# Performance work log

Hardware: AMD Instinct MI355X
Metric: run time of the kernel (lower is better)

The kernel has to match this reference:

```python
import jax, jax.numpy as jnp
import numpy as np

B, L, C = 4, 4096, 2048
NH, K = 32, 16
F = C // NH  # head_dim = 64
LR = 1.0     # config.inner_net_lr
EPS = 1e-6


def setup_inputs() -> dict:
    key = jax.random.key(0)
    ks = jax.random.split(key, 8)
    s = 0.02
    return {
        "hidden_states": jax.random.normal(ks[0], (B, L, C), jnp.float32),
        "q_w": jax.random.normal(ks[1], (C, C), jnp.float32) * s,
        "k_w": jax.random.normal(ks[2], (C, C), jnp.float32) * s,
        "v_w": jax.random.normal(ks[3], (C, C), jnp.float32) * s,
        "o_w": jax.random.normal(ks[4], (C, C), jnp.float32) * s,
        "lin_w": jax.random.normal(ks[5], (NH, 1, C), jnp.float32) * s,
        "lin_b": jnp.zeros((NH, 1), jnp.float32),
        "ln_w": jnp.ones((NH, F), jnp.float32),
        "ln_b": jnp.zeros((NH, F), jnp.float32),
        "W1": jax.random.normal(ks[6], (NH, F, F), jnp.float32) * s,
        "b1": jnp.zeros((NH, 1, F), jnp.float32),
    }


def _ln(z, g, b):
    # LayerNormFunction.forward over last dim (head_dim)
    mu = z.mean(-1, keepdims=True)
    var = jnp.mean((z - mu) ** 2, axis=-1, keepdims=True)
    x_hat = (z - mu) * jax.lax.rsqrt(var + EPS)
    return g * x_hat + b


def _ln_l2_bwd(z, target, g, b):
    # decoder_ln_bwd: grad of 0.5*||LN(z) - target||^2 w.r.t. z, fused LN fwd+bwd
    mu = z.mean(-1, keepdims=True)
    var = jnp.mean((z - mu) ** 2, axis=-1, keepdims=True)
    std = jnp.sqrt(var + EPS)
    x_hat = (z - mu) / std
    gy = (g * x_hat + b - target) * g  # grad_x_hat
    return (F * gy - gy.sum(-1, keepdims=True)
            - x_hat * (gy * x_hat).sum(-1, keepdims=True)) / (F * std)


def reference(hidden_states, q_w, k_w, v_w, o_w, lin_w, lin_b, ln_w, ln_b, W1, b1):
    nc = L // K  # number of inner chunks

    def proj(w):
        x = hidden_states @ w.T                      # [B,L,C]
        x = x.reshape(B, nc, K, NH, F)
        return jnp.moveaxis(x, 3, 1)                 # [B,NH,nc,K,F]

    XC, XB, XA = proj(q_w), proj(k_w), proj(v_w)

    # per-head ilr gate: vmap(F.linear) over heads, softplus activation
    Xr = hidden_states.reshape(B, nc, K, C)
    ilr = jax.nn.softplus(jnp.einsum('bnkc,hoc->bhnko', Xr, lin_w)
                          + lin_b[None, :, None, None, :])   # [B,NH,nc,K,1]
    token_idx = 1.0 / jnp.arange(1, K + 1, dtype=jnp.float32)
    coeff = (LR * token_idx)[None, None, None, :, None] * ilr / F  # [B,NH,nc,K,1]

    gamma = ln_w[None, :, None, :]  # [1,NH,1,F]
    beta = ln_b[None, :, None, :]
    mask = jnp.tril(jnp.ones((K, K), jnp.float32))

    W1_0 = jnp.broadcast_to(W1[None], (B, NH, F, F))
    b1_0 = jnp.broadcast_to(b1[None], (B, NH, 1, F))

    def step(carry, xs):
        W1s, b1s = carry
        xa, xb, xc, co = xs                 # [B,NH,K,F], co: [B,NH,K,1]
        Z1 = xb @ W1s + b1s                 # inner-net forward
        gZ = _ln_l2_bwd(Z1, xa - xb, gamma, beta)  # grad_l_wrt_Z1
        Attn1 = (xc @ jnp.swapaxes(xb, -1, -2)) * mask      # tril(XC XB^T) [B,NH,K,K]
        b1_bar = b1s - (co * mask) @ gZ                      # [B,NH,K,F]
        Z1_bar = xc @ W1s - (co * Attn1) @ gZ + b1_bar       # dual-form output
        co_last = co[:, :, -1:, :]                           # [B,NH,1,1]
        W1_new = W1s - jnp.swapaxes(co_last * xb, -1, -2) @ gZ
        b1_new = b1_bar[:, :, -1:, :]
        xcw = xc + _ln(Z1_bar, gamma, beta)
        return (W1_new, b1_new), xcw

    xs = tuple(jnp.moveaxis(t, 2, 0) for t in (XA, XB, XC, coeff))
    _, out = jax.lax.scan(step, (W1_0, b1_0), xs)   # out: [nc,B,NH,K,F]
    out = jnp.moveaxis(out, 0, 1)                    # [B,nc,NH,K,F]
    out = jnp.swapaxes(out, 2, 3).reshape(B, L, C)   # [B,L,C]
    return out @ o_w.T
```

## Files before the change

kernel.cpp:

```cpp
#include <hip/hip_runtime.h>
#include <hip/hip_bf16.h>

#define B_ 4
#define L_ 4096
#define C_ 2048
#define NH_ 32
#define K_ 16
#define F_ 64
#define NC_ 256
#define EPS_ 1e-6f

typedef _Float16 half8 __attribute__((ext_vector_type(8)));
typedef _Float16 half4 __attribute__((ext_vector_type(4)));
typedef float f32x4 __attribute__((ext_vector_type(4)));

__device__ __forceinline__ float red16(float v) {
  int x;
  x = __builtin_amdgcn_update_dpp(0, __builtin_bit_cast(int, v), 0xB1, 0xF, 0xF, true);
  v += __builtin_bit_cast(float, x);
  x = __builtin_amdgcn_update_dpp(0, __builtin_bit_cast(int, v), 0x4E, 0xF, 0xF, true);
  v += __builtin_bit_cast(float, x);
  x = __builtin_amdgcn_update_dpp(0, __builtin_bit_cast(int, v), 0x124, 0xF, 0xF, true);
  v += __builtin_bit_cast(float, x);
  x = __builtin_amdgcn_update_dpp(0, __builtin_bit_cast(int, v), 0x128, 0xF, 0xF, true);
  v += __builtin_bit_cast(float, x);
  return v;
}

__device__ __forceinline__ void gl_lds16(const _Float16* g, _Float16* l) {
  __builtin_amdgcn_global_load_lds(
      (const __attribute__((address_space(1))) void*)g,
      (__attribute__((address_space(3))) void*)l, 16, 0, 0);
}

__global__ __launch_bounds__(256) void cast_f16(const float* __restrict__ in,
                                                _Float16* __restrict__ out, int n8) {
  int i = blockIdx.x * 256 + threadIdx.x;
  if (i >= n8) return;
  const float4* ip = (const float4*)in;
  float4 a = ip[2*i], b = ip[2*i+1];
  half8 o;
  o[0]=(_Float16)a.x; o[1]=(_Float16)a.y; o[2]=(_Float16)a.z; o[3]=(_Float16)a.w;
  o[4]=(_Float16)b.x; o[5]=(_Float16)b.y; o[6]=(_Float16)b.z; o[7]=(_Float16)b.w;
  ((half8*)out)[i] = o;
}

#define TM 128
#define TN 128
#define TK 32

template<typename OT>
__global__ __launch_bounds__(256) void gemm_f16(
    const _Float16* __restrict__ A, const _Float16* __restrict__ Bm,
    OT* __restrict__ C, int M, int N, int Kd)
{
  __shared__ __align__(16) _Float16 As[TM*TK];
  __shared__ __align__(16) _Float16 Bs[TN*TK];
  const int t = threadIdx.x;
  const int lane = t & 63;
  const int bn = blockIdx.x, bm = blockIdx.y;
  const int w = t >> 6;
  const int wm = (w >> 1) * 64, wn = (w & 1) * 64;

  const _Float16* ga1 = A  + ((long)(bm*TM +      (t>>2)))*Kd + (t&3)*8;
  const _Float16* ga2 = A  + ((long)(bm*TM + 64 + (t>>2)))*Kd + (t&3)*8;
  const _Float16* gb1 = Bm + ((long)(bn*TN +      (t>>2)))*Kd + (t&3)*8;
  const _Float16* gb2 = Bm + ((long)(bn*TN + 64 + (t>>2)))*Kd + (t&3)*8;
  _Float16* la1 = As + (size_t)t*8;
  _Float16* la2 = As + (size_t)(t+256)*8;
  _Float16* lb1 = Bs + (size_t)t*8;
  _Float16* lb2 = Bs + (size_t)(t+256)*8;

  f32x4 acc[4][4];
#pragma unroll
  for (int i = 0; i < 4; ++i)
#pragma unroll
    for (int j = 0; j < 4; ++j) acc[i][j] = (f32x4){0.f,0.f,0.f,0.f};

  for (int k0 = 0; k0 < Kd; k0 += TK) {
    __syncthreads();
    gl_lds16(ga1 + k0, la1);
    gl_lds16(ga2 + k0, la2);
    gl_lds16(gb1 + k0, lb1);
    gl_lds16(gb2 + k0, lb2);
    __syncthreads();
    half8 af[4], bf[4];
#pragma unroll
    for (int i = 0; i < 4; ++i)
      af[i] = *(const half8*)(As + (size_t)(wm + i*16 + (lane&15))*TK + (lane>>4)*8);
#pragma unroll
    for (int j = 0; j < 4; ++j)
      bf[j] = *(const half8*)(Bs + (size_t)(wn + j*16 + (lane&15))*TK + (lane>>4)*8);
#pragma unroll
    for (int i = 0; i < 4; ++i)
#pragma unroll
      for (int j = 0; j < 4; ++j)
        acc[i][j] = __builtin_amdgcn_mfma_f32_16x16x32_f16(af[i], bf[j], acc[i][j], 0, 0, 0);
  }

  const int cr = (lane >> 4) * 4, cc = lane & 15;
#pragma unroll
  for (int i = 0; i < 4; ++i)
#pragma unroll
    for (int j = 0; j < 4; ++j)
#pragma unroll
      for (int r = 0; r < 4; ++r) {
        long row = (long)bm*TM + wm + i*16 + cr + r;
        long col = (long)bn*TN + wn + j*16 + cc;
        C[row*(long)N + col] = (OT)acc[i][j][r];
      }
}

__global__ __launch_bounds__(256) void ilr_kernel(
    const float* __restrict__ hid, const float* __restrict__ lin_w,
    const float* __restrict__ lin_b, float* __restrict__ coeff)
{
  const int t = threadIdx.x;
  const int lane = t & 63;
  const int w = t >> 6;
  const int row0 = blockIdx.x * 16 + w * 4;

  float4 hv[4][8];
#pragma unroll
  for (int r = 0; r < 4; ++r) {
    const float* hp = hid + (size_t)(row0 + r) * C_;
#pragma unroll
    for (int i = 0; i < 8; ++i) hv[r][i] = *(const float4*)(hp + i*256 + lane*4);
  }
  float res[4] = {0.f,0.f,0.f,0.f};
  for (int h = 0; h < NH_; ++h) {
    const float* wp = lin_w + (size_t)h * C_;
    float s[4] = {0.f,0.f,0.f,0.f};
#pragma unroll
    for (int i = 0; i < 8; ++i) {
      float4 wv = *(const float4*)(wp + i*256 + lane*4);
#pragma unroll
      for (int r = 0; r < 4; ++r)
        s[r] += hv[r][i].x*wv.x + hv[r][i].y*wv.y + hv[r][i].z*wv.z + hv[r][i].w*wv.w;
    }
#pragma unroll
    for (int o = 32; o > 0; o >>= 1)
#pragma unroll
      for (int r = 0; r < 4; ++r) s[r] += __shfl_xor(s[r], o, 64);
    if (lane == h) { res[0]=s[0]; res[1]=s[1]; res[2]=s[2]; res[3]=s[3]; }
  }
  if (lane < NH_) {
    float lb = lin_b[lane];
#pragma unroll
    for (int r = 0; r < 4; ++r) {
      int row = row0 + r;
      int b = row >> 12;
      int li = row & (L_ - 1);
      int k = li & (K_ - 1);
      float x = res[r] + lb;
      float sp = (x > 20.f) ? x : log1pf(expf(x));
      float v = (1.0f / (float)(k + 1)) * sp * (1.0f / (float)F_);
      coeff[((size_t)(b * NH_ + lane)) * L_ + li] = v;
    }
  }
}


struct Ck {
  half4 xbA[4], xcA[4], xaA[4];
  float co4[4], co15;
};

__device__ __forceinline__ void load_ck(
    Ck& c, const _Float16* Q, const _Float16* Kp, const _Float16* V,
    const float* co, size_t rowbase, int hoff, size_t cobase, int n, int q, int ln)
{
#pragma unroll
  for (int kt = 0; kt < 4; ++kt) {
    size_t idx = (rowbase + ln) * C_ + hoff + 16*kt + 4*q;
    c.xbA[kt] = *(const half4*)(Kp + idx);
    c.xcA[kt] = *(const half4*)(Q  + idx);
    c.xaA[kt] = *(const half4*)(V  + idx);
  }
#pragma unroll
  for (int r = 0; r < 4; ++r) c.co4[r] = co[cobase + (size_t)n*K_ + 4*q + r];
  c.co15 = co[cobase + (size_t)n*K_ + 15];
}

__global__ __launch_bounds__(64, 1) void scan_kernel(
    const _Float16* __restrict__ Q, const _Float16* __restrict__ Kp,
    const _Float16* __restrict__ V,
    const float* __restrict__ coeff, const float* __restrict__ W1g, const float* __restrict__ b1g,
    const float* __restrict__ ln_w, const float* __restrict__ ln_b,
    _Float16* __restrict__ OF)
{
  const int bh = blockIdx.x;
  const int b = bh >> 5, h = bh & 31;
  const int lane = threadIdx.x;
  const int q = lane >> 4, ln = lane & 15;
  const int hoff = h * F_;
  const size_t cobase = (size_t)bh * L_;
  const size_t brow = (size_t)b * L_;

  half4 Whi[4][4];
  f32x4 Wlo[4][4];
#pragma unroll
  for (int kt = 0; kt < 4; ++kt)
#pragma unroll
    for (int t = 0; t < 4; ++t) {
      half4 hv; f32x4 lv;
#pragma unroll
      for (int j = 0; j < 4; ++j) {
        float wv = W1g[(size_t)h*F_*F_ + (size_t)(16*kt + 4*q + j)*F_ + 16*t + ln];
        _Float16 hi = (_Float16)wv;
        hv[j] = hi; lv[j] = wv - (float)hi;
      }
      Whi[kt][t] = hv; Wlo[kt][t] = lv;
    }
  float b1r[4], gamt[4], bett[4];
#pragma unroll
  for (int t = 0; t < 4; ++t) {
    b1r[t]  = b1g[hoff + 16*t + ln];
    gamt[t] = ln_w[hoff + 16*t + ln];
    bett[t] = ln_b[hoff + 16*t + ln];
  }
  half4 maskA, maskI;
#pragma unroll
  for (int j = 0; j < 4; ++j) {
    maskA[j] = (_Float16)((4*q + j <= ln) ? 1.f : 0.f);
    maskI[j] = (_Float16)((4*q + j == ln) ? 1.f : 0.f);
  }
  const f32x4 zf4 = (f32x4){0.f, 0.f, 0.f, 0.f};

  auto body = [&](const Ck& ck, int n) {
    const size_t rowbase = brow + (size_t)n * K_;

    half4 Wlo16[4][4];
#pragma unroll
    for (int kt = 0; kt < 4; ++kt)
#pragma unroll
      for (int t = 0; t < 4; ++t) {
        half4 lv;
#pragma unroll
        for (int j = 0; j < 4; ++j) lv[j] = (_Float16)Wlo[kt][t][j];
        Wlo16[kt][t] = lv;
      }

    f32x4 tgD[4], xcsD[4];
    half4 xbT[4];
#pragma unroll
    for (int t = 0; t < 4; ++t) {
      half4 dd = ck.xaA[t] - ck.xbA[t];
      tgD[t]  = __builtin_amdgcn_mfma_f32_16x16x16f16(dd, maskI, zf4, 0, 0, 0);
      xcsD[t] = __builtin_amdgcn_mfma_f32_16x16x16f16(ck.xcA[t], maskI, zf4, 0, 0, 0);
      f32x4 x = __builtin_amdgcn_mfma_f32_16x16x16f16(ck.xbA[t], maskI, zf4, 0, 0, 0);
      half4 v;
#pragma unroll
      for (int r = 0; r < 4; ++r) v[r] = (_Float16)x[r];
      xbT[t] = v;
    }

    f32x4 za[4];
#pragma unroll
    for (int t = 0; t < 4; ++t) {
      f32x4 zh = (f32x4){b1r[t], b1r[t], b1r[t], b1r[t]};
      f32x4 zl = zf4;
#pragma unroll
      for (int kt = 0; kt < 4; ++kt) {
        zh = __builtin_amdgcn_mfma_f32_16x16x16f16(ck.xbA[kt], Whi[kt][t],   zh, 0, 0, 0);
        zl = __builtin_amdgcn_mfma_f32_16x16x16f16(ck.xbA[kt], Wlo16[kt][t], zl, 0, 0, 0);
      }
      za[t] = zh + zl;
    }

    f32x4 at0 = zf4, at1 = zf4;
    at0 = __builtin_amdgcn_mfma_f32_16x16x16f16(ck.xbA[0], ck.xcA[0], at0, 0, 0, 0);
    at0 = __builtin_amdgcn_mfma_f32_16x16x16f16(ck.xbA[1], ck.xcA[1], at0, 0, 0, 0);
    at1 = __builtin_amdgcn_mfma_f32_16x16x16f16(ck.xbA[2], ck.xcA[2], at1, 0, 0, 0);
    at1 = __builtin_amdgcn_mfma_f32_16x16x16f16(ck.xbA[3], ck.xcA[3], at1, 0, 0, 0);
    f32x4 at = at0 + at1;
    half4 atf;
#pragma unroll
    for (int r = 0; r < 4; ++r) atf[r] = (_Float16)((4*q + r <= ln) ? at[r] : 0.f);

    half4 gzf[4];
#pragma unroll
    for (int r = 0; r < 4; ++r) {
      float zr[4], s1 = 0.f, s2 = 0.f;
#pragma unroll
      for (int t = 0; t < 4; ++t) { zr[t] = za[t][r]; s1 += zr[t]; s2 += zr[t]*zr[t]; }
      s1 = red16(s1); s2 = red16(s2);
      float mu = s1 * (1.f/F_);
      float istd = rsqrtf(s2 * (1.f/F_) - mu*mu + EPS_);
      float xh[4], gy[4], sg = 0.f, sx = 0.f;
#pragma unroll
      for (int t = 0; t < 4; ++t) {
        xh[t] = (zr[t] - mu) * istd;
        gy[t] = (gamt[t]*xh[t] + bett[t] - tgD[t][r]) * gamt[t];
        sg += gy[t]; sx += gy[t]*xh[t];
      }
      sg = red16(sg); sx = red16(sx);
      const float sc = istd * (1.f/F_);
#pragma unroll
      for (int t = 0; t < 4; ++t)
        gzf[t][r] = (_Float16)((F_*gy[t] - sg - xh[t]*sx) * sc);
    }

    f32x4 cum[4], ag[4];
#pragma unroll
    for (int t = 0; t < 4; ++t) {
      cum[t] = __builtin_amdgcn_mfma_f32_16x16x16f16(maskA, gzf[t], zf4, 0, 0, 0);
      ag[t]  = __builtin_amdgcn_mfma_f32_16x16x16f16(atf,   gzf[t], zf4, 0, 0, 0);
    }

    float zbf[4][4];
#pragma unroll
    for (int t = 0; t < 4; ++t) {
      f32x4 zh = zf4, zl = zf4;
#pragma unroll
      for (int kt = 0; kt < 4; ++kt) {
        zh = __builtin_amdgcn_mfma_f32_16x16x16f16(ck.xcA[kt], Whi[kt][t],   zh, 0, 0, 0);
        zl = __builtin_amdgcn_mfma_f32_16x16x16f16(ck.xcA[kt], Wlo16[kt][t], zl, 0, 0, 0);
      }
      f32x4 s = zh + zl;
#pragma unroll
      for (int r = 0; r < 4; ++r)
        zbf[t][r] = s[r] + b1r[t] - ck.co4[r]*(ag[t][r] + cum[t][r]);
    }

#pragma unroll
    for (int r = 0; r < 4; ++r) {
      float zr[4], s1 = 0.f, s2 = 0.f;
#pragma unroll
      for (int t = 0; t < 4; ++t) { zr[t] = zbf[t][r]; s1 += zr[t]; s2 += zr[t]*zr[t]; }
      s1 = red16(s1); s2 = red16(s2);
      float mu = s1 * (1.f/F_);
      float istd = rsqrtf(s2 * (1.f/F_) - mu*mu + EPS_);
#pragma unroll
      for (int t = 0; t < 4; ++t) {
        float ov = xcsD[t][r] + gamt[t]*((zr[t] - mu)*istd) + bett[t];
        OF[(rowbase + 4*q + r) * C_ + hoff + 16*t + ln] = (_Float16)ov;
      }
    }

#pragma unroll
    for (int t = 0; t < 4; ++t) {
      float tmp = b1r[t] - ck.co15 * cum[t][3];
      b1r[t] = __shfl(tmp, 48 + ln, 64);
    }

#pragma unroll
    for (int mt = 0; mt < 4; ++mt)
#pragma unroll
      for (int t = 0; t < 4; ++t) {
        f32x4 d = __builtin_amdgcn_mfma_f32_16x16x16f16(xbT[mt], gzf[t], zf4, 0, 0, 0);
#pragma unroll
        for (int r = 0; r < 4; ++r) Wlo[mt][t][r] -= ck.co15 * d[r];
      }
  };

  Ck cka, ckb;
  load_ck(cka, Q, Kp, V, coeff, brow, hoff, cobase, 0, q, ln);
  for (int n = 0; n < NC_; n += 2) {
    load_ck(ckb, Q, Kp, V, coeff, brow + (size_t)(n+1)*K_, hoff, cobase, n+1, q, ln);
    body(cka, n);
    int np = (n + 2 < NC_) ? n + 2 : NC_ - 1;
    load_ck(cka, Q, Kp, V, coeff, brow + (size_t)np*K_, hoff, cobase, np, q, ln);
    body(ckb, n + 1);
  }
}

extern "C" void kernel_launch(void* const* d_in, const int* in_sizes, int n_in,
                              void* d_out, int out_size, void* d_ws, size_t ws_size,
                              hipStream_t stream)
{
  const float* hid   = (const float*)d_in[0];
  const float* q_w   = (const float*)d_in[1];
  const float* k_w   = (const float*)d_in[2];
  const float* v_w   = (const float*)d_in[3];
  const float* o_w   = (const float*)d_in[4];
  const float* lin_w = (const float*)d_in[5];
  const float* lin_b = (const float*)d_in[6];
  const float* ln_w  = (const float*)d_in[7];
  const float* ln_b  = (const float*)d_in[8];
  const float* W1    = (const float*)d_in[9];
  const float* b1    = (const float*)d_in[10];
  float* out = (float*)d_out;

  const size_t BLC = (size_t)B_ * L_ * C_;
  const size_t CC  = (size_t)C_ * C_;
  _Float16* HF = (_Float16*)d_ws;
  _Float16* WF = HF + BLC;
  _Float16* KF = WF + CC;
  _Float16* VF = KF + BLC;
  float*    CO = (float*)(VF + BLC);
  _Float16* QF = (_Float16*)d_out;

  const int M = B_ * L_, N = C_, Kd = C_;
  dim3 gg(N / TN, M / TM);
  const int n8h = (int)(BLC / 8);
  const int n8w = (int)(CC / 8);

  cast_f16<<<(n8h+255)/256, 256, 0, stream>>>(hid, HF, n8h);
  cast_f16<<<(n8w+255)/256, 256, 0, stream>>>(q_w, WF, n8w);
  gemm_f16<_Float16><<<gg, 256, 0, stream>>>(HF, WF, QF, M, N, Kd);
  cast_f16<<<(n8w+255)/256, 256, 0, stream>>>(k_w, WF, n8w);
  gemm_f16<_Float16><<<gg, 256, 0, stream>>>(HF, WF, KF, M, N, Kd);
  cast_f16<<<(n8w+255)/256, 256, 0, stream>>>(v_w, WF, n8w);
  gemm_f16<_Float16><<<gg, 256, 0, stream>>>(HF, WF, VF, M, N, Kd);
  ilr_kernel<<<M / 16, 256, 0, stream>>>(hid, lin_w, lin_b, CO);
  scan_kernel<<<B_ * NH_, 64, 0, stream>>>(QF, KF, VF, CO, W1, b1, ln_w, ln_b, HF);
  cast_f16<<<(n8w+255)/256, 256, 0, stream>>>(o_w, WF, n8w);
  gemm_f16<float><<<gg, 256, 0, stream>>>(HF, WF, out, M, N, Kd);
}
```

Baseline: 1.517 ms.

## Split scan into producer/consumer waves pipelined one chunk apart via LDS

```diff
diff --git a/kernel.cpp b/kernel.cpp
--- a/kernel.cpp
+++ b/kernel.cpp
@@ -161,28 +161,27 @@
 }
 
 
-struct Ck {
-  half4 xbA[4], xcA[4], xaA[4];
+struct Ck2 {
+  half4 xbA[4], xsA[4];
   float co4[4], co15;
 };
 
-__device__ __forceinline__ void load_ck(
-    Ck& c, const _Float16* Q, const _Float16* Kp, const _Float16* V,
-    const float* co, size_t rowbase, int hoff, size_t cobase, int n, int q, int ln)
+__device__ __forceinline__ void load_ck2(
+    Ck2& c, const _Float16* Kp, const _Float16* S, const float* co,
+    size_t rowbase, int hoff, size_t cobase, int n, int q, int ln)
 {
 #pragma unroll
   for (int kt = 0; kt < 4; ++kt) {
     size_t idx = (rowbase + ln) * C_ + hoff + 16*kt + 4*q;
     c.xbA[kt] = *(const half4*)(Kp + idx);
-    c.xcA[kt] = *(const half4*)(Q  + idx);
-    c.xaA[kt] = *(const half4*)(V  + idx);
+    c.xsA[kt] = *(const half4*)(S  + idx);
   }
 #pragma unroll
   for (int r = 0; r < 4; ++r) c.co4[r] = co[cobase + (size_t)n*K_ + 4*q + r];
   c.co15 = co[cobase + (size_t)n*K_ + 15];
 }
 
-__global__ __launch_bounds__(64, 1) void scan_kernel(
+__global__ __launch_bounds__(128, 1) void scan_kernel(
     const _Float16* __restrict__ Q, const _Float16* __restrict__ Kp,
     const _Float16* __restrict__ V,
     const float* __restrict__ coeff, const float* __restrict__ W1g, const float* __restrict__ b1g,
@@ -191,11 +190,15 @@
 {
   const int bh = blockIdx.x;
   const int b = bh >> 5, h = bh & 31;
-  const int lane = threadIdx.x;
+  const int tid = threadIdx.x;
+  const int lane = tid & 63;
+  const bool isP = tid < 64;
   const int q = lane >> 4, ln = lane & 15;
   const int hoff = h * F_;
   const size_t cobase = (size_t)bh * L_;
   const size_t brow = (size_t)b * L_;
+
+  __shared__ half4 gzs[4][4][64];
 
   half4 Whi[4][4];
   f32x4 Wlo[4][4];
@@ -227,142 +230,197 @@
   }
   const f32x4 zf4 = (f32x4){0.f, 0.f, 0.f, 0.f};
 
-  auto body = [&](const Ck& ck, int n) {
-    const size_t rowbase = brow + (size_t)n * K_;
-
-    half4 Wlo16[4][4];
-#pragma unroll
-    for (int kt = 0; kt < 4; ++kt)
-#pragma unroll
-      for (int t = 0; t < 4; ++t) {
-        half4 lv;
-#pragma unroll
-        for (int j = 0; j < 4; ++j) lv[j] = (_Float16)Wlo[kt][t][j];
-        Wlo16[kt][t] = lv;
+  const _Float16* S = isP ? V : Q;
+
+  auto iter = [&](int i, Ck2& cur, Ck2& nxt) {
+    half4 gzf[4];
+    half4 xbTp[4];
+    float co15p = 0.f;
+
+    if (isP) {
+      if (i < NC_) {
+        co15p = cur.co15;
+        if (i + 1 < NC_)
+          load_ck2(nxt, Kp, S, coeff, brow + (size_t)(i+1)*K_, hoff, cobase, i+1, q, ln);
+        half4 Wlo16[4][4];
+#pragma unroll
+        for (int kt = 0; kt < 4; ++kt)
+#pragma unroll
+          for (int t = 0; t < 4; ++t) {
+            half4 lv;
+#pragma unroll
+            for (int j = 0; j < 4; ++j) lv[j] = (_Float16)Wlo[kt][t][j];
+            Wlo16[kt][t] = lv;
+          }
+        f32x4 tgD[4];
+#pragma unroll
+        for (int t = 0; t < 4; ++t) {
+          half4 dd = cur.xsA[t] - cur.xbA[t];
+          tgD[t] = __builtin_amdgcn_mfma_f32_16x16x16f16(dd, maskI, zf4, 0, 0, 0);
+          f32x4 x = __builtin_amdgcn_mfma_f32_16x16x16f16(cur.xbA[t], maskI, zf4, 0, 0, 0);
+          half4 v;
+#pragma unroll
+          for (int r = 0; r < 4; ++r) v[r] = (_Float16)x[r];
+          xbTp[t] = v;
+        }
+        f32x4 za[4];
+#pragma unroll
+        for (int t = 0; t < 4; ++t) {
+          f32x4 zh = (f32x4){b1r[t], b1r[t], b1r[t], b1r[t]};
+          f32x4 zl = zf4;
+#pragma unroll
+          for (int kt = 0; kt < 4; ++kt) {
+            zh = __builtin_amdgcn_mfma_f32_16x16x16f16(cur.xbA[kt], Whi[kt][t],   zh, 0, 0, 0);
+            zl = __builtin_amdgcn_mfma_f32_16x16x16f16(cur.xbA[kt], Wlo16[kt][t], zl, 0, 0, 0);
+          }
+          za[t] = zh + zl;
+        }
+#pragma unroll
+        for (int r = 0; r < 4; ++r) {
+          float zr[4], s1 = 0.f, s2 = 0.f;
+#pragma unroll
+          for (int t = 0; t < 4; ++t) { zr[t] = za[t][r]; s1 += zr[t]; s2 += zr[t]*zr[t]; }
+          s1 = red16(s1); s2 = red16(s2);
+          float mu = s1 * (1.f/F_);
+          float istd = rsqrtf(s2 * (1.f/F_) - mu*mu + EPS_);
+          float xh[4], gy[4], sg = 0.f, sx = 0.f;
+#pragma unroll
+          for (int t = 0; t < 4; ++t) {
+            xh[t] = (zr[t] - mu) * istd;
+            gy[t] = (gamt[t]*xh[t] + bett[t] - tgD[t][r]) * gamt[t];
+            sg += gy[t]; sx += gy[t]*xh[t];
+          }
+          sg = red16(sg); sx = red16(sx);
+          const float sc = istd * (1.f/F_);
+#pragma unroll
+          for (int t = 0; t < 4; ++t)
+            gzf[t][r] = (_Float16)((F_*gy[t] - sg - xh[t]*sx) * sc);
+        }
+#pragma unroll
+        for (int t = 0; t < 4; ++t) gzs[i & 3][t][lane] = gzf[t];
       }
-
-    f32x4 tgD[4], xcsD[4];
-    half4 xbT[4];
-#pragma unroll
-    for (int t = 0; t < 4; ++t) {
-      half4 dd = ck.xaA[t] - ck.xbA[t];
-      tgD[t]  = __builtin_amdgcn_mfma_f32_16x16x16f16(dd, maskI, zf4, 0, 0, 0);
-      xcsD[t] = __builtin_amdgcn_mfma_f32_16x16x16f16(ck.xcA[t], maskI, zf4, 0, 0, 0);
-      f32x4 x = __builtin_amdgcn_mfma_f32_16x16x16f16(ck.xbA[t], maskI, zf4, 0, 0, 0);
-      half4 v;
-#pragma unroll
-      for (int r = 0; r < 4; ++r) v[r] = (_Float16)x[r];
-      xbT[t] = v;
+    } else {
+      if (i < NC_)
+        load_ck2(nxt, Kp, S, coeff, brow + (size_t)i*K_, hoff, cobase, i, q, ln);
     }
 
-    f32x4 za[4];
-#pragma unroll
-    for (int t = 0; t < 4; ++t) {
-      f32x4 zh = (f32x4){b1r[t], b1r[t], b1r[t], b1r[t]};
-      f32x4 zl = zf4;
-#pragma unroll
-      for (int kt = 0; kt < 4; ++kt) {
-        zh = __builtin_amdgcn_mfma_f32_16x16x16f16(ck.xbA[kt], Whi[kt][t],   zh, 0, 0, 0);
-        zl = __builtin_amdgcn_mfma_f32_16x16x16f16(ck.xbA[kt], Wlo16[kt][t], zl, 0, 0, 0);
+    __syncthreads();
+
+    if (isP) {
+      if (i < NC_) {
+        f32x4 cum3[4];
+#pragma unroll
+        for (int t = 0; t < 4; ++t)
+          cum3[t] = __builtin_amdgcn_mfma_f32_16x16x16f16(maskA, gzf[t], zf4, 0, 0, 0);
+#pragma unroll
+        for (int t = 0; t < 4; ++t) {
+          float tmp = b1r[t] - co15p * cum3[t][3];
+          b1r[t] = __shfl(tmp, 48 + ln, 64);
+        }
+#pragma unroll
+        for (int mt = 0; mt < 4; ++mt)
+#pragma unroll
+          for (int t = 0; t < 4; ++t) {
+            f32x4 d = __builtin_amdgcn_mfma_f32_16x16x16f16(xbTp[mt], gzf[t], zf4, 0, 0, 0);
+#pragma unroll
+            for (int r = 0; r < 4; ++r) Wlo[mt][t][r] -= co15p * d[r];
+          }
       }
-      za[t] = zh + zl;
-    }
-
-    f32x4 at0 = zf4, at1 = zf4;
-    at0 = __builtin_amdgcn_mfma_f32_16x16x16f16(ck.xbA[0], ck.xcA[0], at0, 0, 0, 0);
-    at0 = __builtin_amdgcn_mfma_f32_16x16x16f16(ck.xbA[1], ck.xcA[1], at0, 0, 0, 0);
-    at1 = __builtin_amdgcn_mfma_f32_16x16x16f16(ck.xbA[2], ck.xcA[2], at1, 0, 0, 0);
-    at1 = __builtin_amdgcn_mfma_f32_16x16x16f16(ck.xbA[3], ck.xcA[3], at1, 0, 0, 0);
-    f32x4 at = at0 + at1;
-    half4 atf;
-#pragma unroll
-    for (int r = 0; r < 4; ++r) atf[r] = (_Float16)((4*q + r <= ln) ? at[r] : 0.f);
-
-    half4 gzf[4];
-#pragma unroll
-    for (int r = 0; r < 4; ++r) {
-      float zr[4], s1 = 0.f, s2 = 0.f;
-#pragma unroll
-      for (int t = 0; t < 4; ++t) { zr[t] = za[t][r]; s1 += zr[t]; s2 += zr[t]*zr[t]; }
-      s1 = red16(s1); s2 = red16(s2);
-      float mu = s1 * (1.f/F_);
-      float istd = rsqrtf(s2 * (1.f/F_) - mu*mu + EPS_);
-      float xh[4], gy[4], sg = 0.f, sx = 0.f;
-#pragma unroll
-      for (int t = 0; t < 4; ++t) {
-        xh[t] = (zr[t] - mu) * istd;
-        gy[t] = (gamt[t]*xh[t] + bett[t] - tgD[t][r]) * gamt[t];
-        sg += gy[t]; sx += gy[t]*xh[t];
-      }
-      sg = red16(sg); sx = red16(sx);
-      const float sc = istd * (1.f/F_);
-#pragma unroll
-      for (int t = 0; t < 4; ++t)
-        gzf[t][r] = (_Float16)((F_*gy[t] - sg - xh[t]*sx) * sc);
-    }
-
-    f32x4 cum[4], ag[4];
-#pragma unroll
-    for (int t = 0; t < 4; ++t) {
-      cum[t] = __builtin_amdgcn_mfma_f32_16x16x16f16(maskA, gzf[t], zf4, 0, 0, 0);
-      ag[t]  = __builtin_amdgcn_mfma_f32_16x16x16f16(atf,   gzf[t], zf4, 0, 0, 0);
-    }
-
-    float zbf[4][4];
-#pragma unroll
-    for (int t = 0; t < 4; ++t) {
-      f32x4 zh = zf4, zl = zf4;
-#pragma unroll
-      for (int kt = 0; kt < 4; ++kt) {
-        zh = __builtin_amdgcn_mfma_f32_16x16x16f16(ck.xcA[kt], Whi[kt][t],   zh, 0, 0, 0);
-        zl = __builtin_amdgcn_mfma_f32_16x16x16f16(ck.xcA[kt], Wlo16[kt][t], zl, 0, 0, 0);
-      }
-      f32x4 s = zh + zl;
-#pragma unroll
-      for (int r = 0; r < 4; ++r)
-        zbf[t][r] = s[r] + b1r[t] - ck.co4[r]*(ag[t][r] + cum[t][r]);
-    }
-
-#pragma unroll
-    for (int r = 0; r < 4; ++r) {
-      float zr[4], s1 = 0.f, s2 = 0.f;
-#pragma unroll
-      for (int t = 0; t < 4; ++t) { zr[t] = zbf[t][r]; s1 += zr[t]; s2 += zr[t]*zr[t]; }
-      s1 = red16(s1); s2 = red16(s2);
-      float mu = s1 * (1.f/F_);
-      float istd = rsqrtf(s2 * (1.f/F_) - mu*mu + EPS_);
-#pragma unroll
-      for (int t = 0; t < 4; ++t) {
-        float ov = xcsD[t][r] + gamt[t]*((zr[t] - mu)*istd) + bett[t];
-        OF[(rowbase + 4*q + r) * C_ + hoff + 16*t + ln] = (_Float16)ov;
+    } else {
+      if (i > 0) {
+        const int jc = i - 1;
+        const size_t rowbase = brow + (size_t)jc * K_;
+        half4 gz[4];
+#pragma unroll
+        for (int t = 0; t < 4; ++t) gz[t] = gzs[jc & 3][t][lane];
+        f32x4 xcsD[4]; half4 xbT[4];
+#pragma unroll
+        for (int t = 0; t < 4; ++t) {
+          xcsD[t] = __builtin_amdgcn_mfma_f32_16x16x16f16(cur.xsA[t], maskI, zf4, 0, 0, 0);
+          f32x4 x = __builtin_amdgcn_mfma_f32_16x16x16f16(cur.xbA[t], maskI, zf4, 0, 0, 0);
+          half4 v;
+#pragma unroll
+          for (int r = 0; r < 4; ++r) v[r] = (_Float16)x[r];
+          xbT[t] = v;
+        }
+        f32x4 at0 = zf4, at1 = zf4;
+        at0 = __builtin_amdgcn_mfma_f32_16x16x16f16(cur.xbA[0], cur.xsA[0], at0, 0, 0, 0);
+        at0 = __builtin_amdgcn_mfma_f32_16x16x16f16(cur.xbA[1], cur.xsA[1], at0, 0, 0, 0);
+        at1 = __builtin_amdgcn_mfma_f32_16x16x16f16(cur.xbA[2], cur.xsA[2], at1, 0, 0, 0);
+        at1 = __builtin_amdgcn_mfma_f32_16x16x16f16(cur.xbA[3], cur.xsA[3], at1, 0, 0, 0);
+        f32x4 at = at0 + at1;
+        half4 atf;
+#pragma unroll
+        for (int r = 0; r < 4; ++r) atf[r] = (_Float16)((4*q + r <= ln) ? at[r] : 0.f);
+        f32x4 cum[4], ag[4];
+#pragma unroll
+        for (int t = 0; t < 4; ++t) {
+          cum[t] = __builtin_amdgcn_mfma_f32_16x16x16f16(maskA, gz[t], zf4, 0, 0, 0);
+          ag[t]  = __builtin_amdgcn_mfma_f32_16x16x16f16(atf,   gz[t], zf4, 0, 0, 0);
+        }
+        half4 Wlo16[4][4];
+#pragma unroll
+        for (int kt = 0; kt < 4; ++kt)
+#pragma unroll
+          for (int t = 0; t < 4; ++t) {
+            half4 lv;
+#pragma unroll
+            for (int j = 0; j < 4; ++j) lv[j] = (_Float16)Wlo[kt][t][j];
+            Wlo16[kt][t] = lv;
+          }
+        float zbf[4][4];
+#pragma unroll
+        for (int t = 0; t < 4; ++t) {
+          f32x4 zh = zf4, zl = zf4;
+#pragma unroll
+          for (int kt = 0; kt < 4; ++kt) {
+            zh = __builtin_amdgcn_mfma_f32_16x16x16f16(cur.xsA[kt], Whi[kt][t],   zh, 0, 0, 0);
+            zl = __builtin_amdgcn_mfma_f32_16x16x16f16(cur.xsA[kt], Wlo16[kt][t], zl, 0, 0, 0);
+          }
+          f32x4 s = zh + zl;
+#pragma unroll
+          for (int r = 0; r < 4; ++r)
+            zbf[t][r] = s[r] + b1r[t] - cur.co4[r]*(ag[t][r] + cum[t][r]);
+        }
+#pragma unroll
+        for (int r = 0; r < 4; ++r) {
+          float zr[4], s1 = 0.f, s2 = 0.f;
+#pragma unroll
+          for (int t = 0; t < 4; ++t) { zr[t] = zbf[t][r]; s1 += zr[t]; s2 += zr[t]*zr[t]; }
+          s1 = red16(s1); s2 = red16(s2);
+          float mu = s1 * (1.f/F_);
+          float istd = rsqrtf(s2 * (1.f/F_) - mu*mu + EPS_);
+#pragma unroll
+          for (int t = 0; t < 4; ++t) {
+            float ov = xcsD[t][r] + gamt[t]*((zr[t] - mu)*istd) + bett[t];
+            OF[(rowbase + 4*q + r) * C_ + hoff + 16*t + ln] = (_Float16)ov;
+          }
+        }
+#pragma unroll
+        for (int t = 0; t < 4; ++t) {
+          float tmp = b1r[t] - cur.co15 * cum[t][3];
+          b1r[t] = __shfl(tmp, 48 + ln, 64);
+        }
+#pragma unroll
+        for (int mt = 0; mt < 4; ++mt)
+#pragma unroll
+          for (int t = 0; t < 4; ++t) {
+            f32x4 d = __builtin_amdgcn_mfma_f32_16x16x16f16(xbT[mt], gz[t], zf4, 0, 0, 0);
+#pragma unroll
+            for (int r = 0; r < 4; ++r) Wlo[mt][t][r] -= cur.co15 * d[r];
+          }
       }
     }
-
-#pragma unroll
-    for (int t = 0; t < 4; ++t) {
-      float tmp = b1r[t] - ck.co15 * cum[t][3];
-      b1r[t] = __shfl(tmp, 48 + ln, 64);
-    }
-
-#pragma unroll
-    for (int mt = 0; mt < 4; ++mt)
-#pragma unroll
-      for (int t = 0; t < 4; ++t) {
-        f32x4 d = __builtin_amdgcn_mfma_f32_16x16x16f16(xbT[mt], gzf[t], zf4, 0, 0, 0);
-#pragma unroll
-        for (int r = 0; r < 4; ++r) Wlo[mt][t][r] -= ck.co15 * d[r];
-      }
   };
 
-  Ck cka, ckb;
-  load_ck(cka, Q, Kp, V, coeff, brow, hoff, cobase, 0, q, ln);
-  for (int n = 0; n < NC_; n += 2) {
-    load_ck(ckb, Q, Kp, V, coeff, brow + (size_t)(n+1)*K_, hoff, cobase, n+1, q, ln);
-    body(cka, n);
-    int np = (n + 2 < NC_) ? n + 2 : NC_ - 1;
-    load_ck(cka, Q, Kp, V, coeff, brow + (size_t)np*K_, hoff, cobase, np, q, ln);
-    body(ckb, n + 1);
-  }
+  Ck2 cka, ckb;
+  if (isP) load_ck2(cka, Kp, S, coeff, brow, hoff, cobase, 0, q, ln);
+
+  for (int i = 0; i < NC_; i += 2) {
+    iter(i,     cka, ckb);
+    iter(i + 1, ckb, cka);
+  }
+  iter(NC_, cka, ckb);
 }
 
 extern "C" void kernel_launch(void* const* d_in, const int* in_sizes, int n_in,
@@ -404,7 +462,7 @@
   cast_f16<<<(n8w+255)/256, 256, 0, stream>>>(v_w, WF, n8w);
   gemm_f16<_Float16><<<gg, 256, 0, stream>>>(HF, WF, VF, M, N, Kd);
   ilr_kernel<<<M / 16, 256, 0, stream>>>(hid, lin_w, lin_b, CO);
-  scan_kernel<<<B_ * NH_, 64, 0, stream>>>(QF, KF, VF, CO, W1, b1, ln_w, ln_b, HF);
+  scan_kernel<<<B_ * NH_, 128, 0, stream>>>(QF, KF, VF, CO, W1, b1, ln_w, ln_b, HF);
   cast_f16<<<(n8w+255)/256, 256, 0, stream>>>(o_w, WF, n8w);
   gemm_f16<float><<<gg, 256, 0, stream>>>(HF, WF, out, M, N, Kd);
 }
```

Result: faster. 1.433 ms (-5.5%).

## Process two heads per wave in scan kernel and keep W1 low part in fp16

Applied to the files above, without the earlier changes.

```diff
diff --git a/kernel.cpp b/kernel.cpp
--- a/kernel.cpp
+++ b/kernel.cpp
@@ -189,36 +189,39 @@
     const float* __restrict__ ln_w, const float* __restrict__ ln_b,
     _Float16* __restrict__ OF)
 {
-  const int bh = blockIdx.x;
-  const int b = bh >> 5, h = bh & 31;
+  const int bh0 = blockIdx.x * 2;
+  const int b = bh0 >> 5;
   const int lane = threadIdx.x;
   const int q = lane >> 4, ln = lane & 15;
-  const int hoff = h * F_;
-  const size_t cobase = (size_t)bh * L_;
+  const int hoffA[2]    = {(bh0 & 31) * F_, ((bh0 & 31) + 1) * F_};
+  const size_t cobaseA[2] = {(size_t)bh0 * L_, (size_t)(bh0 + 1) * L_};
   const size_t brow = (size_t)b * L_;
 
-  half4 Whi[4][4];
-  f32x4 Wlo[4][4];
-#pragma unroll
-  for (int kt = 0; kt < 4; ++kt)
+  half4 Whi[2][4][4], Wlo16[2][4][4];
+#pragma unroll
+  for (int hh = 0; hh < 2; ++hh)
+#pragma unroll
+    for (int kt = 0; kt < 4; ++kt)
+#pragma unroll
+      for (int t = 0; t < 4; ++t) {
+        half4 hv, lv;
+#pragma unroll
+        for (int j = 0; j < 4; ++j) {
+          float wv = W1g[(size_t)((bh0 & 31) + hh)*F_*F_ + (size_t)(16*kt + 4*q + j)*F_ + 16*t + ln];
+          _Float16 hi = (_Float16)wv;
+          hv[j] = hi; lv[j] = (_Float16)(wv - (float)hi);
+        }
+        Whi[hh][kt][t] = hv; Wlo16[hh][kt][t] = lv;
+      }
+  float b1r[2][4], gamt[2][4], bett[2][4];
+#pragma unroll
+  for (int hh = 0; hh < 2; ++hh)
 #pragma unroll
     for (int t = 0; t < 4; ++t) {
-      half4 hv; f32x4 lv;
-#pragma unroll
-      for (int j = 0; j < 4; ++j) {
-        float wv = W1g[(size_t)h*F_*F_ + (size_t)(16*kt + 4*q + j)*F_ + 16*t + ln];
-        _Float16 hi = (_Float16)wv;
-        hv[j] = hi; lv[j] = wv - (float)hi;
-      }
-      Whi[kt][t] = hv; Wlo[kt][t] = lv;
+      b1r[hh][t]  = b1g[hoffA[hh] + 16*t + ln];
+      gamt[hh][t] = ln_w[hoffA[hh] + 16*t + ln];
+      bett[hh][t] = ln_b[hoffA[hh] + 16*t + ln];
     }
-  float b1r[4], gamt[4], bett[4];
-#pragma unroll
-  for (int t = 0; t < 4; ++t) {
-    b1r[t]  = b1g[hoff + 16*t + ln];
-    gamt[t] = ln_w[hoff + 16*t + ln];
-    bett[t] = ln_b[hoff + 16*t + ln];
-  }
   half4 maskA, maskI;
 #pragma unroll
   for (int j = 0; j < 4; ++j) {
@@ -227,141 +230,157 @@
   }
   const f32x4 zf4 = (f32x4){0.f, 0.f, 0.f, 0.f};
 
-  auto body = [&](const Ck& ck, int n) {
+  auto body2 = [&](const Ck* ck, int n) {
     const size_t rowbase = brow + (size_t)n * K_;
 
-    half4 Wlo16[4][4];
-#pragma unroll
-    for (int kt = 0; kt < 4; ++kt)
-#pragma unroll
-      for (int t = 0; t < 4; ++t) {
-        half4 lv;
-#pragma unroll
-        for (int j = 0; j < 4; ++j) lv[j] = (_Float16)Wlo[kt][t][j];
-        Wlo16[kt][t] = lv;
-      }
-
-    f32x4 tgD[4], xcsD[4];
-    half4 xbT[4];
-#pragma unroll
-    for (int t = 0; t < 4; ++t) {
-      half4 dd = ck.xaA[t] - ck.xbA[t];
-      tgD[t]  = __builtin_amdgcn_mfma_f32_16x16x16f16(dd, maskI, zf4, 0, 0, 0);
-      xcsD[t] = __builtin_amdgcn_mfma_f32_16x16x16f16(ck.xcA[t], maskI, zf4, 0, 0, 0);
-      f32x4 x = __builtin_amdgcn_mfma_f32_16x16x16f16(ck.xbA[t], maskI, zf4, 0, 0, 0);
-      half4 v;
-#pragma unroll
-      for (int r = 0; r < 4; ++r) v[r] = (_Float16)x[r];
-      xbT[t] = v;
+    f32x4 tgD[2][4], xcsD[2][4];
+    half4 xbT[2][4];
+#pragma unroll
+    for (int hh = 0; hh < 2; ++hh)
+#pragma unroll
+      for (int t = 0; t < 4; ++t) {
+        half4 dd = ck[hh].xaA[t] - ck[hh].xbA[t];
+        tgD[hh][t]  = __builtin_amdgcn_mfma_f32_16x16x16f16(dd, maskI, zf4, 0, 0, 0);
+        xcsD[hh][t] = __builtin_amdgcn_mfma_f32_16x16x16f16(ck[hh].xcA[t], maskI, zf4, 0, 0, 0);
+        f32x4 x = __builtin_amdgcn_mfma_f32_16x16x16f16(ck[hh].xbA[t], maskI, zf4, 0, 0, 0);
+        half4 v;
+#pragma unroll
+        for (int r = 0; r < 4; ++r) v[r] = (_Float16)x[r];
+        xbT[hh][t] = v;
+      }
+
+    f32x4 za[2][4];
+#pragma unroll
+    for (int hh = 0; hh < 2; ++hh)
+#pragma unroll
+      for (int t = 0; t < 4; ++t) {
+        f32x4 zh = (f32x4){b1r[hh][t], b1r[hh][t], b1r[hh][t], b1r[hh][t]};
+        f32x4 zl = zf4;
+#pragma unroll
+        for (int kt = 0; kt < 4; ++kt) {
+          zh = __builtin_amdgcn_mfma_f32_16x16x16f16(ck[hh].xbA[kt], Whi[hh][kt][t],   zh, 0, 0, 0);
+          zl = __builtin_amdgcn_mfma_f32_16x16x16f16(ck[hh].xbA[kt], Wlo16[hh][kt][t], zl, 0, 0, 0);
+        }
+        za[hh][t] = zh + zl;
+      }
+
+    half4 atf[2];
+#pragma unroll
+    for (int hh = 0; hh < 2; ++hh) {
+      f32x4 at0 = zf4, at1 = zf4;
+      at0 = __builtin_amdgcn_mfma_f32_16x16x16f16(ck[hh].xbA[0], ck[hh].xcA[0], at0, 0, 0, 0);
+      at0 = __builtin_amdgcn_mfma_f32_16x16x16f16(ck[hh].xbA[1], ck[hh].xcA[1], at0, 0, 0, 0);
+      at1 = __builtin_amdgcn_mfma_f32_16x16x16f16(ck[hh].xbA[2], ck[hh].xcA[2], at1, 0, 0, 0);
+      at1 = __builtin_amdgcn_mfma_f32_16x16x16f16(ck[hh].xbA[3], ck[hh].xcA[3], at1, 0, 0, 0);
+      f32x4 at = at0 + at1;
+#pragma unroll
+      for (int r = 0; r < 4; ++r) atf[hh][r] = (_Float16)((4*q + r <= ln) ? at[r] : 0.f);
     }
 
-    f32x4 za[4];
-#pragma unroll
-    for (int t = 0; t < 4; ++t) {
-      f32x4 zh = (f32x4){b1r[t], b1r[t], b1r[t], b1r[t]};
-      f32x4 zl = zf4;
-#pragma unroll
-      for (int kt = 0; kt < 4; ++kt) {
-        zh = __builtin_amdgcn_mfma_f32_16x16x16f16(ck.xbA[kt], Whi[kt][t],   zh, 0, 0, 0);
-        zl = __builtin_amdgcn_mfma_f32_16x16x16f16(ck.xbA[kt], Wlo16[kt][t], zl, 0, 0, 0);
-      }
-      za[t] = zh + zl;
-    }
-
-    f32x4 at0 = zf4, at1 = zf4;
-    at0 = __builtin_amdgcn_mfma_f32_16x16x16f16(ck.xbA[0], ck.xcA[0], at0, 0, 0, 0);
-    at0 = __builtin_amdgcn_mfma_f32_16x16x16f16(ck.xbA[1], ck.xcA[1], at0, 0, 0, 0);
-    at1 = __builtin_amdgcn_mfma_f32_16x16x16f16(ck.xbA[2], ck.xcA[2], at1, 0, 0, 0);
-    at1 = __builtin_amdgcn_mfma_f32_16x16x16f16(ck.xbA[3], ck.xcA[3], at1, 0, 0, 0);
-    f32x4 at = at0 + at1;
-    half4 atf;
-#pragma unroll
-    for (int r = 0; r < 4; ++r) atf[r] = (_Float16)((4*q + r <= ln) ? at[r] : 0.f);
-
-    half4 gzf[4];
-#pragma unroll
-    for (int r = 0; r < 4; ++r) {
-      float zr[4], s1 = 0.f, s2 = 0.f;
-#pragma unroll
-      for (int t = 0; t < 4; ++t) { zr[t] = za[t][r]; s1 += zr[t]; s2 += zr[t]*zr[t]; }
-      s1 = red16(s1); s2 = red16(s2);
-      float mu = s1 * (1.f/F_);
-      float istd = rsqrtf(s2 * (1.f/F_) - mu*mu + EPS_);
-      float xh[4], gy[4], sg = 0.f, sx = 0.f;
-#pragma unroll
-      for (int t = 0; t < 4; ++t) {
-        xh[t] = (zr[t] - mu) * istd;
-        gy[t] = (gamt[t]*xh[t] + bett[t] - tgD[t][r]) * gamt[t];
-        sg += gy[t]; sx += gy[t]*xh[t];
-      }
-      sg = red16(sg); sx = red16(sx);
-      const float sc = istd * (1.f/F_);
-#pragma unroll
-      for (int t = 0; t < 4; ++t)
-        gzf[t][r] = (_Float16)((F_*gy[t] - sg - xh[t]*sx) * sc);
-    }
-
-    f32x4 cum[4], ag[4];
-#pragma unroll
-    for (int t = 0; t < 4; ++t) {
-      cum[t] = __builtin_amdgcn_mfma_f32_16x16x16f16(maskA, gzf[t], zf4, 0, 0, 0);
-      ag[t]  = __builtin_amdgcn_mfma_f32_16x16x16f16(atf,   gzf[t], zf4, 0, 0, 0);
-    }
-
-    float zbf[4][4];
-#pragma unroll
-    for (int t = 0; t < 4; ++t) {
-      f32x4 zh = zf4, zl = zf4;
-#pragma unroll
-      for (int kt = 0; kt < 4; ++kt) {
-        zh = __builtin_amdgcn_mfma_f32_16x16x16f16(ck.xcA[kt], Whi[kt][t],   zh, 0, 0, 0);
-        zl = __builtin_amdgcn_mfma_f32_16x16x16f16(ck.xcA[kt], Wlo16[kt][t], zl, 0, 0, 0);
-      }
-      f32x4 s = zh + zl;
-#pragma unroll
-      for (int r = 0; r < 4; ++r)
-        zbf[t][r] = s[r] + b1r[t] - ck.co4[r]*(ag[t][r] + cum[t][r]);
-    }
-
-#pragma unroll
-    for (int r = 0; r < 4; ++r) {
-      float zr[4], s1 = 0.f, s2 = 0.f;
-#pragma unroll
-      for (int t = 0; t < 4; ++t) { zr[t] = zbf[t][r]; s1 += zr[t]; s2 += zr[t]*zr[t]; }
-      s1 = red16(s1); s2 = red16(s2);
-      float mu = s1 * (1.f/F_);
-      float istd = rsqrtf(s2 * (1.f/F_) - mu*mu + EPS_);
-#pragma unroll
-      for (int t = 0; t < 4; ++t) {
-        float ov = xcsD[t][r] + gamt[t]*((zr[t] - mu)*istd) + bett[t];
-        OF[(rowbase + 4*q + r) * C_ + hoff + 16*t + ln] = (_Float16)ov;
-      }
-    }
-
-#pragma unroll
-    for (int t = 0; t < 4; ++t) {
-      float tmp = b1r[t] - ck.co15 * cum[t][3];
-      b1r[t] = __shfl(tmp, 48 + ln, 64);
-    }
-
-#pragma unroll
-    for (int mt = 0; mt < 4; ++mt)
-#pragma unroll
-      for (int t = 0; t < 4; ++t) {
-        f32x4 d = __builtin_amdgcn_mfma_f32_16x16x16f16(xbT[mt], gzf[t], zf4, 0, 0, 0);
-#pragma unroll
-        for (int r = 0; r < 4; ++r) Wlo[mt][t][r] -= ck.co15 * d[r];
-      }
+    half4 gzf[2][4];
+#pragma unroll
+    for (int hh = 0; hh < 2; ++hh)
+#pragma unroll
+      for (int r = 0; r < 4; ++r) {
+        float zr[4], s1 = 0.f, s2 = 0.f;
+#pragma unroll
+        for (int t = 0; t < 4; ++t) { zr[t] = za[hh][t][r]; s1 += zr[t]; s2 += zr[t]*zr[t]; }
+        s1 = red16(s1); s2 = red16(s2);
+        float mu = s1 * (1.f/F_);
+        float istd = rsqrtf(s2 * (1.f/F_) - mu*mu + EPS_);
+        float xh[4], gy[4], sg = 0.f, sx = 0.f;
+#pragma unroll
+        for (int t = 0; t < 4; ++t) {
+          xh[t] = (zr[t] - mu) * istd;
+          gy[t] = (gamt[hh][t]*xh[t] + bett[hh][t] - tgD[hh][t][r]) * gamt[hh][t];
+          sg += gy[t]; sx += gy[t]*xh[t];
+        }
+        sg = red16(sg); sx = red16(sx);
+        const float sc = istd * (1.f/F_);
+#pragma unroll
+        for (int t = 0; t < 4; ++t)
+          gzf[hh][t][r] = (_Float16)((F_*gy[t] - sg - xh[t]*sx) * sc);
+      }
+
+    f32x4 cum[2][4], ag[2][4];
+#pragma unroll
+    for (int hh = 0; hh < 2; ++hh)
+#pragma unroll
+      for (int t = 0; t < 4; ++t) {
+        cum[hh][t] = __builtin_amdgcn_mfma_f32_16x16x16f16(maskA, gzf[hh][t], zf4, 0, 0, 0);
+        ag[hh][t]  = __builtin_amdgcn_mfma_f32_16x16x16f16(atf[hh], gzf[hh][t], zf4, 0, 0, 0);
+      }
+
+    float zbf[2][4][4];
+#pragma unroll
+    for (int hh = 0; hh < 2; ++hh)
+#pragma unroll
+      for (int t = 0; t < 4; ++t) {
+        f32x4 zh = zf4, zl = zf4;
+#pragma unroll
+        for (int kt = 0; kt < 4; ++kt) {
+          zh = __builtin_amdgcn_mfma_f32_16x16x16f16(ck[hh].xcA[kt], Whi[hh][kt][t],   zh, 0, 0, 0);
+          zl = __builtin_amdgcn_mfma_f32_16x16x16f16(ck[hh].xcA[kt], Wlo16[hh][kt][t], zl, 0, 0, 0);
+        }
+        f32x4 s = zh + zl;
+#pragma unroll
+        for (int r = 0; r < 4; ++r)
+          zbf[hh][t][r] = s[r] + b1r[hh][t] - ck[hh].co4[r]*(ag[hh][t][r] + cum[hh][t][r]);
+      }
+
+#pragma unroll
+    for (int hh = 0; hh < 2; ++hh)
+#pragma unroll
+      for (int r = 0; r < 4; ++r) {
+        float zr[4], s1 = 0.f, s2 = 0.f;
+#pragma unroll
+        for (int t = 0; t < 4; ++t) { zr[t] = zbf[hh][t][r]; s1 += zr[t]; s2 += zr[t]*zr[t]; }
+        s1 = red16(s1); s2 = red16(s2);
+        float mu = s1 * (1.f/F_);
+        float istd = rsqrtf(s2 * (1.f/F_) - mu*mu + EPS_);
+#pragma unroll
+        for (int t = 0; t < 4; ++t) {
+          float ov = xcsD[hh][t][r] + gamt[hh][t]*((zr[t] - mu)*istd) + bett[hh][t];
+          OF[(rowbase + 4*q + r) * C_ + hoffA[hh] + 16*t + ln] = (_Float16)ov;
+        }
+      }
+
+#pragma unroll
+    for (int hh = 0; hh < 2; ++hh)
+#pragma unroll
+      for (int t = 0; t < 4; ++t) {
+        float tmp = b1r[hh][t] - ck[hh].co15 * cum[hh][t][3];
+        b1r[hh][t] = __shfl(tmp, 48 + ln, 64);
+      }
+
+#pragma unroll
+    for (int hh = 0; hh < 2; ++hh)
+#pragma unroll
+      for (int mt = 0; mt < 4; ++mt)
+#pragma unroll
+        for (int t = 0; t < 4; ++t) {
+          f32x4 d = __builtin_amdgcn_mfma_f32_16x16x16f16(xbT[hh][mt], gzf[hh][t], zf4, 0, 0, 0);
+          half4 dt;
+#pragma unroll
+          for (int r = 0; r < 4; ++r) dt[r] = (_Float16)(ck[hh].co15 * d[r]);
+          Wlo16[hh][mt][t] = Wlo16[hh][mt][t] - dt;
+        }
   };
 
-  Ck cka, ckb;
-  load_ck(cka, Q, Kp, V, coeff, brow, hoff, cobase, 0, q, ln);
+  Ck cka[2], ckb[2];
+#pragma unroll
+  for (int hh = 0; hh < 2; ++hh)
+    load_ck(cka[hh], Q, Kp, V, coeff, brow, hoffA[hh], cobaseA[hh], 0, q, ln);
   for (int n = 0; n < NC_; n += 2) {
-    load_ck(ckb, Q, Kp, V, coeff, brow + (size_t)(n+1)*K_, hoff, cobase, n+1, q, ln);
-    body(cka, n);
+#pragma unroll
+    for (int hh = 0; hh < 2; ++hh)
+      load_ck(ckb[hh], Q, Kp, V, coeff, brow + (size_t)(n+1)*K_, hoffA[hh], cobaseA[hh], n+1, q, ln);
+    body2(cka, n);
     int np = (n + 2 < NC_) ? n + 2 : NC_ - 1;
-    load_ck(cka, Q, Kp, V, coeff, brow + (size_t)np*K_, hoff, cobase, np, q, ln);
-    body(ckb, n + 1);
+#pragma unroll
+    for (int hh = 0; hh < 2; ++hh)
+      load_ck(cka[hh], Q, Kp, V, coeff, brow + (size_t)np*K_, hoffA[hh], cobaseA[hh], np, q, ln);
+    body2(ckb, n + 1);
   }
 }
 
@@ -404,7 +423,7 @@
   cast_f16<<<(n8w+255)/256, 256, 0, stream>>>(v_w, WF, n8w);
   gemm_f16<_Float16><<<gg, 256, 0, stream>>>(HF, WF, VF, M, N, Kd);
   ilr_kernel<<<M / 16, 256, 0, stream>>>(hid, lin_w, lin_b, CO);
-  scan_kernel<<<B_ * NH_, 64, 0, stream>>>(QF, KF, VF, CO, W1, b1, ln_w, ln_b, HF);
+  scan_kernel<<<B_ * NH_ / 2, 64, 0, stream>>>(QF, KF, VF, CO, W1, b1, ln_w, ln_b, HF);
   cast_f16<<<(n8w+255)/256, 256, 0, stream>>>(o_w, WF, n8w);
   gemm_f16<float><<<gg, 256, 0, stream>>>(HF, WF, out, M, N, Kd);
 }
```

Measured after the change: 2.471 ms. 62.9% more time.
